# Performance work log

Measured on AMD Instinct MI355X. Metric: run time of the kernel, lower is better.

The kernel has to match this reference:

```python
import jax, jax.numpy as jnp
import numpy as np

D, P, H, FF, HD = 1024, 512, 16, 4096, 64
B, L = 2, 1024
EPS = 1e-5


def rotate_half(x):
    x1, x2 = jnp.split(x, 2, axis=-1)
    return jnp.concatenate([-x2, x1], axis=-1)


def apply_rope(x, pos):  # x: [B,H,L,HD], pos: [L,HD] angles
    c = jnp.cos(pos)[None, None]
    s = jnp.sin(pos)[None, None]
    return x * c + rotate_half(x) * s


def layer_norm(x, g, b):
    mu = jnp.mean(x, axis=-1, keepdims=True)
    var = jnp.var(x, axis=-1, keepdims=True)
    return (x - mu) * jax.lax.rsqrt(var + EPS) * g + b


def heads(x):  # [B,L,D] -> [B,H,L,HD]
    Bq, Lq, _ = x.shape
    return x.reshape(Bq, Lq, H, HD).transpose(0, 2, 1, 3)


def attention(q, k, v, alibi, pos, mask):
    if pos is not None:
        q = apply_rope(q, pos)
        k = apply_rope(k, pos)
    scores = jnp.einsum('bhqd,bhkd->bhqk', q, k) * (HD ** -0.5)
    scores = jnp.where(mask[:, None, None, :], -jnp.inf, scores)
    scores = scores + alibi[None]
    w = jax.nn.softmax(scores, axis=-1)
    out = jnp.einsum('bhqk,bhkd->bhqd', w, v)
    return out.transpose(0, 2, 1, 3).reshape(out.shape[0], out.shape[2], D)


def setup_inputs() -> dict:
    key = jax.random.key(0)
    ks = iter(jax.random.split(key, 64))

    def rn(shape, scale=1.0):
        return jax.random.normal(next(ks), shape, dtype=jnp.float32) * scale

    inp = {
        'memory': rn((B, L, D)),
        'tgt': rn((B, L, D)),
        'self_alibi_bias': rn((H, L, L)),
        'self_pos_emb': rn((L, HD)),
        'cross_alibi_bias': rn((H, L, L)),
        'cross_pos_emb': rn((L, HD)),
        'mask': jax.random.randint(next(ks), (B, L), 0, 2) > 0,
        # self attention params
        'sa_lat_w': rn((D, P), 0.02), 'sa_lat_b': jnp.zeros((P,)),
        'sa_q_w': rn((P, D), 0.02), 'sa_q_b': jnp.zeros((D,)),
        'sa_k_w': rn((P, D), 0.02), 'sa_k_b': jnp.zeros((D,)),
        'sa_v_w': rn((P, D), 0.02), 'sa_v_b': jnp.zeros((D,)),
        'sa_out_w': rn((D, D), 0.02), 'sa_out_b': jnp.zeros((D,)),
        # cross attention params
        'ca_lat_w': rn((D, P), 0.02), 'ca_lat_b': jnp.zeros((P,)),
        'ca_q_w': rn((D, D), 0.02), 'ca_q_b': jnp.zeros((D,)),
        'ca_k_w': rn((P, D), 0.02), 'ca_k_b': jnp.zeros((D,)),
        'ca_v_w': rn((P, D), 0.02), 'ca_v_b': jnp.zeros((D,)),
        'ca_out_w': rn((D, D), 0.02), 'ca_out_b': jnp.zeros((D,)),
        # ffn + norms
        'lin1_w': rn((D, FF), 0.02), 'lin1_b': jnp.zeros((FF,)),
        'lin2_w': rn((FF, D), 0.02), 'lin2_b': jnp.zeros((D,)),
        'n1_g': jnp.ones((D,)), 'n1_b': jnp.zeros((D,)),
        'n2_g': jnp.ones((D,)), 'n2_b': jnp.zeros((D,)),
        'n3_g': jnp.ones((D,)), 'n3_b': jnp.zeros((D,)),
    }
    return inp


def reference(memory, tgt, self_alibi_bias, self_pos_emb, cross_alibi_bias,
              cross_pos_emb, mask,
              sa_lat_w, sa_lat_b, sa_q_w, sa_q_b, sa_k_w, sa_k_b,
              sa_v_w, sa_v_b, sa_out_w, sa_out_b,
              ca_lat_w, ca_lat_b, ca_q_w, ca_q_b, ca_k_w, ca_k_b,
              ca_v_w, ca_v_b, ca_out_w, ca_out_b,
              lin1_w, lin1_b, lin2_w, lin2_b,
              n1_g, n1_b, n2_g, n2_b, n3_g, n3_b):
    # self attention (q,k,v all from latent projection of tgt)
    proj = tgt @ sa_lat_w + sa_lat_b                      # [B,L,P]
    q = heads(proj @ sa_q_w + sa_q_b)
    k = heads(proj @ sa_k_w + sa_k_b)
    v = heads(proj @ sa_v_w + sa_v_b)
    sa = attention(q, k, v, self_alibi_bias, self_pos_emb, mask)
    sa = sa @ sa_out_w + sa_out_b
    x = tgt + layer_norm(sa, n1_g, n1_b)

    # cross attention (q from current tgt stream, k/v from latent of memory)
    mproj = memory @ ca_lat_w + ca_lat_b                  # [B,L,P]
    q = heads(x @ ca_q_w + ca_q_b)
    k = heads(mproj @ ca_k_w + ca_k_b)
    v = heads(mproj @ ca_v_w + ca_v_b)
    ca = attention(q, k, v, cross_alibi_bias, cross_pos_emb, mask)
    ca = ca @ ca_out_w + ca_out_b
    x = x + layer_norm(ca, n2_g, n2_b)

    # FFN
    f = jax.nn.gelu(x @ lin1_w + lin1_b, approximate=False) @ lin2_w + lin2_b
    x = layer_norm(x + f, n3_g, n3_b)
    return x
```

## Files before the change

kernel.cpp:

```cpp
#include <hip/hip_runtime.h>
#include <hip/hip_bf16.h>
#include <math.h>

typedef __hip_bfloat16 hbf16;
typedef __attribute__((ext_vector_type(8))) short bf16x8;
typedef __attribute__((ext_vector_type(4))) float f32x4;

constexpr int kD  = 1024;
constexpr int kP  = 512;
constexpr int kH  = 16;
constexpr int kFF = 4096;
constexpr int kHD = 64;
constexpr int kB  = 2;
constexpr int kL  = 1024;
constexpr int kTok = kB * kL;

__device__ inline short f2bf(float x) { hbf16 h = __float2bfloat16(x); return *(short*)&h; }

__device__ __forceinline__ void gload16(const void* g, void* l) {
    __builtin_amdgcn_global_load_lds(
        (const __attribute__((address_space(1))) void*)g,
        (__attribute__((address_space(3))) void*)l, 16, 0, 0);
}

__global__ __launch_bounds__(256) void cast_bf16(
    const float* __restrict__ in, short* __restrict__ out, int total4)
{
    int i = blockIdx.x * 256 + threadIdx.x;
    if (i >= total4) return;
    float4 v = *(const float4*)&in[(size_t)i * 4];
    *(short4*)&out[(size_t)i * 4] = make_short4(f2bf(v.x), f2bf(v.y), f2bf(v.z), f2bf(v.w));
}

__global__ __launch_bounds__(256) void transpose_bf16(
    const float* __restrict__ src, short* __restrict__ dst, int K, int N)
{
    __shared__ float t[32][33];
    int n0 = blockIdx.x * 32, k0 = blockIdx.y * 32;
    int tx = threadIdx.x & 31, ty = threadIdx.x >> 5;
    #pragma unroll
    for (int r = ty; r < 32; r += 8)
        t[r][tx] = src[(size_t)(k0 + r) * N + n0 + tx];
    __syncthreads();
    #pragma unroll
    for (int r = ty; r < 32; r += 8)
        dst[(size_t)(n0 + r) * K + k0 + tx] = f2bf(t[tx][r]);
}

__global__ __launch_bounds__(256) void bias_fill(
    const float* __restrict__ bias, float* __restrict__ C, int N, int total4)
{
    int i = blockIdx.x * 256 + threadIdx.x;
    if (i >= total4) return;
    int n = (i * 4) & (N - 1);
    *(float4*)&C[(size_t)i * 4] = *(const float4*)&bias[n];
}

__global__ void concat_bias(float* __restrict__ o, const float* __restrict__ a,
                            const float* __restrict__ b, const float* __restrict__ c, int n)
{
    int i = blockIdx.x * blockDim.x + threadIdx.x;
    if (i < n) o[i] = a[i];
    else if (i < 2 * n) { if (b) o[i] = b[i - n]; }
    else if (i < 3 * n) { if (c) o[i] = c[i - 2 * n]; }
}

__global__ __launch_bounds__(256) void gemm_mfma(
    const short* __restrict__ A, const short* __restrict__ WT,
    const float* __restrict__ bias, float* __restrict__ C, short* __restrict__ C16,
    int M, int N, int K, int act, int ksplit)
{
    __shared__ short As[128 * 32];
    __shared__ short Bs[128 * 32];
    const int tid = threadIdx.x;

    const int gx = gridDim.x;
    const int nwg = gx * gridDim.y;
    const int orig = blockIdx.y * gx + blockIdx.x;
    const int qq = nwg >> 3, rr = nwg & 7;
    const int xcd = orig & 7, lid = orig >> 3;
    const int swz = (xcd < rr) ? (xcd * (qq + 1) + lid)
                               : (rr * (qq + 1) + (xcd - rr) * qq + lid);
    const int m0 = (swz / gx) * 128, n0 = (swz % gx) * 128;

    const int ks = K / ksplit;
    const int kbeg = blockIdx.z * ks, kend = kbeg + ks;
    const int wave = tid >> 6, lane = tid & 63;
    const int l15 = lane & 15, quad = lane >> 4;
    const int wm = (wave & 1) * 64, wn = (wave >> 1) * 64;

    const int srow = wave * 32 + (lane >> 2);
    const int scol = (lane & 3) * 8;

    f32x4 acc[4][4];
    #pragma unroll
    for (int i = 0; i < 4; ++i)
        #pragma unroll
        for (int j = 0; j < 4; ++j)
            acc[i][j] = (f32x4){0.f, 0.f, 0.f, 0.f};

    for (int kk = kbeg; kk < kend; kk += 32) {
        gload16(&A [(size_t)(m0 + srow) * K + kk + scol],      &As[wave * 1024]);
        gload16(&A [(size_t)(m0 + srow + 16) * K + kk + scol], &As[wave * 1024 + 512]);
        gload16(&WT[(size_t)(n0 + srow) * K + kk + scol],      &Bs[wave * 1024]);
        gload16(&WT[(size_t)(n0 + srow + 16) * K + kk + scol], &Bs[wave * 1024 + 512]);
        __syncthreads();

        bf16x8 af[4], bfr[4];
        #pragma unroll
        for (int i = 0; i < 4; ++i)
            af[i] = *(bf16x8*)&As[(wm + i * 16 + l15) * 32 + quad * 8];
        #pragma unroll
        for (int j = 0; j < 4; ++j)
            bfr[j] = *(bf16x8*)&Bs[(wn + j * 16 + l15) * 32 + quad * 8];
        #pragma unroll
        for (int i = 0; i < 4; ++i)
            #pragma unroll
            for (int j = 0; j < 4; ++j)
                acc[i][j] = __builtin_amdgcn_mfma_f32_16x16x32_bf16(af[i], bfr[j], acc[i][j], 0, 0, 0);
        __syncthreads();
    }

    #pragma unroll
    for (int j = 0; j < 4; ++j) {
        int n = n0 + wn + j * 16 + l15;
        if (ksplit == 1) {
            float bv = bias[n];
            #pragma unroll
            for (int i = 0; i < 4; ++i) {
                int mb = m0 + wm + i * 16 + quad * 4;
                #pragma unroll
                for (int r = 0; r < 4; ++r) {
                    float v = acc[i][j][r] + bv;
                    if (act) v = v * 0.5f * (1.0f + erff(v * 0.70710678118654752f));
                    if (C)   C[(size_t)(mb + r) * N + n] = v;
                    if (C16) C16[(size_t)(mb + r) * N + n] = f2bf(v);
                }
            }
        } else {
            #pragma unroll
            for (int i = 0; i < 4; ++i) {
                int mb = m0 + wm + i * 16 + quad * 4;
                #pragma unroll
                for (int r = 0; r < 4; ++r)
                    atomicAdd(&C[(size_t)(mb + r) * N + n], acc[i][j][r]);
            }
        }
    }
}

__global__ void qk_pack(const float* __restrict__ x, const float* __restrict__ pos,
                        short* __restrict__ outp, float scale, int ldx, int off)
{
    int idx = blockIdx.x * blockDim.x + threadIdx.x;
    if (idx >= kTok * kH * 32) return;
    int d = idx & 31;
    int h = (idx >> 5) & (kH - 1);
    int row = idx >> 9;
    int l = row & (kL - 1);
    int b = row >> 10;
    float a1 = pos[l * kHD + d];
    float a2 = pos[l * kHD + d + 32];
    size_t base = (size_t)row * ldx + off + h * kHD;
    float x1 = x[base + d], x2 = x[base + d + 32];
    float r1 = (x1 * cosf(a1) - x2 * sinf(a1)) * scale;
    float r2 = (x2 * cosf(a2) + x1 * sinf(a2)) * scale;
    size_t ob = ((size_t)(b * kH + h) * kL + l) * 64;
    outp[ob + d]      = f2bf(r1);
    outp[ob + d + 32] = f2bf(r2);
}

__global__ __launch_bounds__(256) void v_pack(const float* __restrict__ v, short* __restrict__ outp,
                                              int ldx, int off)
{
    int l0 = blockIdx.x * 64, h = blockIdx.y, b = blockIdx.z;
    __shared__ float t[64][65];
    int tid = threadIdx.x;
    #pragma unroll
    for (int e = 0; e < 4; ++e) {
        int idx = tid + e * 256;
        int r = idx >> 4, c4 = (idx & 15) * 4;
        const float4 vv = *(const float4*)&v[(size_t)(b * kL + l0 + r) * ldx + off + h * kHD + c4];
        t[r][c4] = vv.x; t[r][c4 + 1] = vv.y; t[r][c4 + 2] = vv.z; t[r][c4 + 3] = vv.w;
    }
    __syncthreads();
    int hd = tid >> 2, seg = (tid & 3) * 16;
    size_t ob = ((size_t)(b * kH + h) * 64 + hd) * kL + l0 + seg;
    short tmp[16];
    #pragma unroll
    for (int i = 0; i < 16; ++i) tmp[i] = f2bf(t[seg + i][hd]);
    #pragma unroll
    for (int i = 0; i < 16; i += 4)
        *(short4*)&outp[ob + i] = make_short4(tmp[i], tmp[i + 1], tmp[i + 2], tmp[i + 3]);
}

constexpr int AQ = 64, AK = 64;
__global__ __launch_bounds__(256, 2) void attn_mfma(
    const short* __restrict__ qpk, const short* __restrict__ kpk,
    const short* __restrict__ vpk, const float* __restrict__ alibi,
    const int* __restrict__ mask, short* __restrict__ out)
{
    const int q0 = blockIdx.x * AQ, h = blockIdx.y, b = blockIdx.z;
    const int tid = threadIdx.x, wave = tid >> 6, lane = tid & 63;
    const int l15 = lane & 15, quad = lane >> 4;
    __shared__ short Qf[4096];
    __shared__ short Kf[4096];
    __shared__ short Vf[4096];
    __shared__ float ALPS[4 * 1088];

    const short* qbase = qpk + ((size_t)(b * kH + h) * kL) * 64;
    const short* kbase = kpk + ((size_t)(b * kH + h) * kL) * 64;
    const short* vbase = vpk + ((size_t)(b * kH + h) * 64) * kL;
    const float* abase = alibi + ((size_t)h * kL + q0) * kL;
    const int*   mbase = mask + b * kL;

    const int sr = tid >> 3, sc8 = (tid & 7) * 8;
    const int sQuad = (sc8 >> 3) & 3, sS = sc8 >> 5;
    const int ar = tid >> 4, ac4 = (tid & 15) * 4;

    #pragma unroll
    for (int e = 0; e < 2; ++e) {
        int r = sr + e * 32;
        int slot = ((r >> 4) * 2 + sS) * 512 + (r & 15) * 32 + sQuad * 8;
        *(bf16x8*)&Qf[slot] = *(const bf16x8*)&qbase[(size_t)(q0 + r) * 64 + sc8];
    }

    bf16x8 rk[2], rv[2];
    float4 ral[4];
    int4 rmk;
    auto load_tile = [&](int k0) {
        #pragma unroll
        for (int e = 0; e < 2; ++e) {
            int r = sr + e * 32;
            rk[e] = *(const bf16x8*)&kbase[(size_t)(k0 + r) * 64 + sc8];
            rv[e] = *(const bf16x8*)&vbase[(size_t)r * kL + k0 + sc8];
        }
        #pragma unroll
        for (int e = 0; e < 4; ++e)
            ral[e] = *(const float4*)&abase[(size_t)(ar + e * 16) * kL + k0 + ac4];
        rmk = *(const int4*)&mbase[k0 + ac4];
    };
    auto store_tile = [&]() {
        #pragma unroll
        for (int e = 0; e < 2; ++e) {
            int r = sr + e * 32;
            int slot = ((r >> 4) * 2 + sS) * 512 + (r & 15) * 32 + sQuad * 8;
            *(bf16x8*)&Kf[slot] = rk[e];
            *(bf16x8*)&Vf[slot] = rv[e];
        }
        #pragma unroll
        for (int e = 0; e < 4; ++e) {
            float4 a = ral[e];
            a.x = rmk.x ? -1e30f : a.x;
            a.y = rmk.y ? -1e30f : a.y;
            a.z = rmk.z ? -1e30f : a.z;
            a.w = rmk.w ? -1e30f : a.w;
            *(float4*)&ALPS[(ar + e * 16) * 68 + ac4] = a;
        }
    };

    float mst[4], lst[4];
    #pragma unroll
    for (int r = 0; r < 4; ++r) { mst[r] = -3e38f; lst[r] = 0.f; }
    f32x4 oacc[4];
    #pragma unroll
    for (int j = 0; j < 4; ++j) oacc[j] = (f32x4){0.f, 0.f, 0.f, 0.f};

    load_tile(0);
    __syncthreads();

    bf16x8 aq[2];
    #pragma unroll
    for (int s = 0; s < 2; ++s)
        aq[s] = *(bf16x8*)&Qf[(wave * 2 + s) * 512 + l15 * 32 + quad * 8];

    for (int t = 0; t < kL / AK; ++t) {
        store_tile();
        __syncthreads();
        if (t + 1 < kL / AK) load_tile((t + 1) * AK);

        f32x4 sacc[4];
        #pragma unroll
        for (int nt = 0; nt < 4; ++nt) sacc[nt] = (f32x4){0.f, 0.f, 0.f, 0.f};
        #pragma unroll
        for (int nt = 0; nt < 4; ++nt)
            #pragma unroll
            for (int s = 0; s < 2; ++s) {
                bf16x8 bk = *(bf16x8*)&Kf[(nt * 2 + s) * 512 + l15 * 32 + quad * 8];
                sacc[nt] = __builtin_amdgcn_mfma_f32_16x16x32_bf16(aq[s], bk, sacc[nt], 0, 0, 0);
            }

        float sv[4][4];
        float mx[4] = {-3e38f, -3e38f, -3e38f, -3e38f};
        #pragma unroll
        for (int nt = 0; nt < 4; ++nt)
            #pragma unroll
            for (int r = 0; r < 4; ++r) {
                float al = ALPS[(wave * 16 + quad * 4 + r) * 68 + nt * 16 + l15];
                float s = sacc[nt][r] + al;
                sv[nt][r] = s;
                mx[r] = fmaxf(mx[r], s);
            }
        #pragma unroll
        for (int m = 1; m <= 8; m <<= 1)
            #pragma unroll
            for (int r = 0; r < 4; ++r)
                mx[r] = fmaxf(mx[r], __shfl_xor(mx[r], m));
        float alpha[4], lsum[4];
        #pragma unroll
        for (int r = 0; r < 4; ++r) {
            float mn = fmaxf(mst[r], mx[r]);
            alpha[r] = __expf(mst[r] - mn);
            mst[r] = mn;
            lsum[r] = 0.f;
        }
        #pragma unroll
        for (int nt = 0; nt < 4; ++nt)
            #pragma unroll
            for (int r = 0; r < 4; ++r) {
                float p = __expf(sv[nt][r] - mst[r]);
                sv[nt][r] = p;
                lsum[r] += p;
            }
        #pragma unroll
        for (int m = 1; m <= 8; m <<= 1)
            #pragma unroll
            for (int r = 0; r < 4; ++r)
                lsum[r] += __shfl_xor(lsum[r], m);
        #pragma unroll
        for (int r = 0; r < 4; ++r) lst[r] = lst[r] * alpha[r] + lsum[r];

        #pragma unroll
        for (int nt = 0; nt < 4; ++nt)
            #pragma unroll
            for (int r = 0; r < 4; ++r)
                ALPS[wave * 1088 + (quad * 4 + r) * 67 + nt * 16 + l15] = sv[nt][r];
        #pragma unroll
        for (int j = 0; j < 4; ++j)
            #pragma unroll
            for (int r = 0; r < 4; ++r)
                oacc[j][r] *= alpha[r];

        #pragma unroll
        for (int s = 0; s < 2; ++s) {
            int pb = wave * 1088 + l15 * 67 + s * 32 + quad * 8;
            bf16x8 ap;
            #pragma unroll
            for (int e = 0; e < 8; ++e) ap[e] = f2bf(ALPS[pb + e]);
            #pragma unroll
            for (int j = 0; j < 4; ++j) {
                bf16x8 bv = *(bf16x8*)&Vf[(j * 2 + s) * 512 + l15 * 32 + quad * 8];
                oacc[j] = __builtin_amdgcn_mfma_f32_16x16x32_bf16(ap, bv, oacc[j], 0, 0, 0);
            }
        }
        __syncthreads();
    }

    #pragma unroll
    for (int j = 0; j < 4; ++j)
        #pragma unroll
        for (int r = 0; r < 4; ++r) {
            int qrow = q0 + wave * 16 + quad * 4 + r;
            out[(size_t)(b * kL + qrow) * kD + h * kHD + j * 16 + l15] = f2bf(oacc[j][r] / lst[r]);
        }
}

__global__ __launch_bounds__(256) void add_ln(
    const float* __restrict__ res, const float* __restrict__ z,
    const float* __restrict__ g, const float* __restrict__ bi,
    float* __restrict__ out, short* __restrict__ out16)
{
    int row = blockIdx.x, tid = threadIdx.x;
    __shared__ float red[256], red2[256];
    const float* zr = z + (size_t)row * kD;
    float s = 0.f, sq = 0.f;
    for (int i = tid; i < kD; i += 256) { float vv = zr[i]; s += vv; sq += vv * vv; }
    red[tid] = s; red2[tid] = sq; __syncthreads();
    for (int st = 128; st > 0; st >>= 1) {
        if (tid < st) { red[tid] += red[tid + st]; red2[tid] += red2[tid + st]; }
        __syncthreads();
    }
    float mean = red[0] / kD;
    float var = red2[0] / kD - mean * mean;
    float rstd = rsqrtf(var + 1e-5f);
    for (int i = tid; i < kD; i += 256) {
        float vv = (zr[i] - mean) * rstd * g[i] + bi[i];
        float o = res[(size_t)row * kD + i] + vv;
        out[(size_t)row * kD + i] = o;
        out16[(size_t)row * kD + i] = f2bf(o);
    }
}

__global__ __launch_bounds__(256) void ln_final(
    const float* __restrict__ res, const float* __restrict__ f,
    const float* __restrict__ g, const float* __restrict__ bi,
    float* __restrict__ out)
{
    int row = blockIdx.x, tid = threadIdx.x;
    __shared__ float tt[kD];
    __shared__ float red[256], red2[256];
    float s = 0.f, sq = 0.f;
    for (int i = tid; i < kD; i += 256) {
        float vv = res[(size_t)row * kD + i] + f[(size_t)row * kD + i];
        tt[i] = vv; s += vv; sq += vv * vv;
    }
    red[tid] = s; red2[tid] = sq; __syncthreads();
    for (int st = 128; st > 0; st >>= 1) {
        if (tid < st) { red[tid] += red[tid + st]; red2[tid] += red2[tid + st]; }
        __syncthreads();
    }
    float mean = red[0] / kD;
    float var = red2[0] / kD - mean * mean;
    float rstd = rsqrtf(var + 1e-5f);
    for (int i = tid; i < kD; i += 256)
        out[(size_t)row * kD + i] = (tt[i] - mean) * rstd * g[i] + bi[i];
}

extern "C" void kernel_launch(void* const* d_in, const int* in_sizes, int n_in,
                              void* d_out, int out_size, void* d_ws, size_t ws_size,
                              hipStream_t stream)
{
    const float* memory      = (const float*)d_in[0];
    const float* tgt         = (const float*)d_in[1];
    const float* self_alibi  = (const float*)d_in[2];
    const float* self_pos    = (const float*)d_in[3];
    const float* cross_alibi = (const float*)d_in[4];
    const float* cross_pos   = (const float*)d_in[5];
    const int*   mask        = (const int*)d_in[6];
    const float* sa_lat_w = (const float*)d_in[7];   const float* sa_lat_b = (const float*)d_in[8];
    const float* sa_q_w   = (const float*)d_in[9];   const float* sa_q_b   = (const float*)d_in[10];
    const float* sa_k_w   = (const float*)d_in[11];  const float* sa_k_b   = (const float*)d_in[12];
    const float* sa_v_w   = (const float*)d_in[13];  const float* sa_v_b   = (const float*)d_in[14];
    const float* sa_out_w = (const float*)d_in[15];  const float* sa_out_b = (const float*)d_in[16];
    const float* ca_lat_w = (const float*)d_in[17];  const float* ca_lat_b = (const float*)d_in[18];
    const float* ca_q_w   = (const float*)d_in[19];  const float* ca_q_b   = (const float*)d_in[20];
    const float* ca_k_w   = (const float*)d_in[21];  const float* ca_k_b   = (const float*)d_in[22];
    const float* ca_v_w   = (const float*)d_in[23];  const float* ca_v_b   = (const float*)d_in[24];
    const float* ca_out_w = (const float*)d_in[25];  const float* ca_out_b = (const float*)d_in[26];
    const float* lin1_w   = (const float*)d_in[27];  const float* lin1_b   = (const float*)d_in[28];
    const float* lin2_w   = (const float*)d_in[29];  const float* lin2_b   = (const float*)d_in[30];
    const float* n1_g = (const float*)d_in[31];  const float* n1_b = (const float*)d_in[32];
    const float* n2_g = (const float*)d_in[33];  const float* n2_b = (const float*)d_in[34];
    const float* n3_g = (const float*)d_in[35];  const float* n3_b = (const float*)d_in[36];

    const size_t M1 = 1u << 20;
    float* W      = (float*)d_ws;
    float* xb     = W;
    short* tgt16  = (short*)W;
    float* tmp    = W + 2 * M1;
    short* mem16  = (short*)(W + 2 * M1);
    short* xb16   = (short*)(W + 4 * M1);
    float* proj   = W + 5 * M1;
    short* qpk    = (short*)(W + 5 * M1);
    short* proj16 = (short*)(W + 6 * M1);
    float* qkvb   = W + 6 * M1 + M1 / 2;
    short* attnb16= (short*)(W + 6 * M1 + M1 / 2);
    short* ffh16  = (short*)(W + 7 * M1 + M1 / 2);
    short* wslot  = (short*)(W + 12 * M1 + M1 / 2);
    short* kpk    = (short*)(W + 12 * M1 + M1 / 2);
    short* vpk    = (short*)(W + 13 * M1 + M1 / 2);
    float* bcat   = W + 14 * M1 + M1 / 2;

    auto gemm = [&](const short* A, const float* Wt, const float* bias, float* C, short* C16,
                    int M, int N, int K, int act, int S) {
        transpose_bf16<<<dim3(N / 32, K / 32), dim3(256), 0, stream>>>(Wt, wslot, K, N);
        if (S > 1)
            bias_fill<<<dim3(M * N / 1024), dim3(256), 0, stream>>>(bias, C, N, M * N / 4);
        gemm_mfma<<<dim3(N / 128, M / 128, S), dim3(256), 0, stream>>>(A, wslot, bias, C, C16, M, N, K, act, S);
    };
    dim3 agrid(kL / AQ, kH, kB);
    dim3 vgrid(kL / 64, kH, kB);
    dim3 tgD(kD / 32, kP / 32);

    cast_bf16<<<dim3(2048), dim3(256), 0, stream>>>(tgt, tgt16, kTok * kD / 4);
    gemm(tgt16, sa_lat_w, sa_lat_b, proj, nullptr, kTok, kP, kD, 0, 4);
    cast_bf16<<<dim3(1024), dim3(256), 0, stream>>>(proj, proj16, kTok * kP / 4);
    transpose_bf16<<<tgD, dim3(256), 0, stream>>>(sa_q_w, wslot, kP, kD);
    transpose_bf16<<<tgD, dim3(256), 0, stream>>>(sa_k_w, wslot + (size_t)kD * kP, kP, kD);
    transpose_bf16<<<tgD, dim3(256), 0, stream>>>(sa_v_w, wslot + (size_t)2 * kD * kP, kP, kD);
    concat_bias<<<dim3(12), dim3(256), 0, stream>>>(bcat, sa_q_b, sa_k_b, sa_v_b, kD);
    gemm_mfma<<<dim3(3 * kD / 128, kTok / 128, 1), dim3(256), 0, stream>>>(
        proj16, wslot, bcat, qkvb, nullptr, kTok, 3 * kD, kP, 0, 1);
    qk_pack<<<dim3(4096), dim3(256), 0, stream>>>(qkvb, self_pos, qpk, 0.125f, 3 * kD, 0);
    qk_pack<<<dim3(4096), dim3(256), 0, stream>>>(qkvb, self_pos, kpk, 1.0f, 3 * kD, kD);
    v_pack<<<vgrid, dim3(256), 0, stream>>>(qkvb, vpk, 3 * kD, 2 * kD);
    attn_mfma<<<agrid, dim3(256), 0, stream>>>(qpk, kpk, vpk, self_alibi, mask, attnb16);
    gemm(attnb16, sa_out_w, sa_out_b, tmp, nullptr, kTok, kD, kD, 0, 2);
    add_ln<<<dim3(kTok), dim3(256), 0, stream>>>(tgt, tmp, n1_g, n1_b, xb, xb16);

    cast_bf16<<<dim3(2048), dim3(256), 0, stream>>>(memory, mem16, kTok * kD / 4);
    gemm(mem16, ca_lat_w, ca_lat_b, proj, nullptr, kTok, kP, kD, 0, 4);
    cast_bf16<<<dim3(1024), dim3(256), 0, stream>>>(proj, proj16, kTok * kP / 4);
    float* qb  = qkvb;
    float* kvb = qkvb + 2 * M1;
    gemm(xb16, ca_q_w, ca_q_b, qb, nullptr, kTok, kD, kD, 0, 2);
    transpose_bf16<<<tgD, dim3(256), 0, stream>>>(ca_k_w, wslot, kP, kD);
    transpose_bf16<<<tgD, dim3(256), 0, stream>>>(ca_v_w, wslot + (size_t)kD * kP, kP, kD);
    concat_bias<<<dim3(8), dim3(256), 0, stream>>>(bcat, ca_k_b, ca_v_b, nullptr, kD);
    gemm_mfma<<<dim3(2 * kD / 128, kTok / 128, 1), dim3(256), 0, stream>>>(
        proj16, wslot, bcat, kvb, nullptr, kTok, 2 * kD, kP, 0, 1);
    qk_pack<<<dim3(4096), dim3(256), 0, stream>>>(qb, cross_pos, qpk, 0.125f, kD, 0);
    qk_pack<<<dim3(4096), dim3(256), 0, stream>>>(kvb, cross_pos, kpk, 1.0f, 2 * kD, 0);
    v_pack<<<vgrid, dim3(256), 0, stream>>>(kvb, vpk, 2 * kD, kD);
    attn_mfma<<<agrid, dim3(256), 0, stream>>>(qpk, kpk, vpk, cross_alibi, mask, attnb16);
    gemm(attnb16, ca_out_w, ca_out_b, tmp, nullptr, kTok, kD, kD, 0, 2);
    add_ln<<<dim3(kTok), dim3(256), 0, stream>>>(xb, tmp, n2_g, n2_b, xb, xb16);

    gemm(xb16, lin1_w, lin1_b, nullptr, ffh16, kTok, kFF, kD, 1, 1);
    gemm(ffh16, lin2_w, lin2_b, tmp, nullptr, kTok, kD, kFF, 0, 4);
    ln_final<<<dim3(kTok), dim3(256), 0, stream>>>(xb, tmp, n3_g, n3_b, (float*)d_out);
}
```

Baseline: 693.7 us.

## Double-buffer GEMM LDS tiles and use fragment-ordered layout for conflict-free reads

The bf16 MFMA GEMM now keeps two LDS buffers and issues global-to-LDS loads for the next k-slice before doing the MFMAs on the current one, so memory latency can overlap with compute and one barrier per iteration is removed. The staging layout is also reorganised so each 16-row group is stored in fragment order, letting every lane read its bf16x8 at a contiguous lane*8 offset to avoid LDS bank conflicts. This doubles LDS usage (32 KB per block), which may reduce occupancy, and it relies on the single remaining barrier to order the buffer reuse correctly.

```diff
diff --git a/kernel.cpp b/kernel.cpp
--- a/kernel.cpp
+++ b/kernel.cpp
@@ -70,8 +70,8 @@
     const float* __restrict__ bias, float* __restrict__ C, short* __restrict__ C16,
     int M, int N, int K, int act, int ksplit)
 {
-    __shared__ short As[128 * 32];
-    __shared__ short Bs[128 * 32];
+    __shared__ short As[2][4096];
+    __shared__ short Bs[2][4096];
     const int tid = threadIdx.x;
 
     const int gx = gridDim.x;
@@ -89,8 +89,12 @@
     const int l15 = lane & 15, quad = lane >> 4;
     const int wm = (wave & 1) * 64, wn = (wave >> 1) * 64;
 
-    const int srow = wave * 32 + (lane >> 2);
-    const int scol = (lane & 3) * 8;
+    const int sgr = lane & 15;
+    const int sgq = (lane >> 4) * 8;
+    const size_t arow0 = (size_t)(m0 + wave * 32 + sgr) * K + sgq;
+    const size_t arow1 = arow0 + (size_t)16 * K;
+    const size_t brow0 = (size_t)(n0 + wave * 32 + sgr) * K + sgq;
+    const size_t brow1 = brow0 + (size_t)16 * K;
 
     f32x4 acc[4][4];
     #pragma unroll
@@ -99,26 +103,37 @@
         for (int j = 0; j < 4; ++j)
             acc[i][j] = (f32x4){0.f, 0.f, 0.f, 0.f};
 
+    gload16(&A [arow0 + kbeg], &As[0][(wave * 2) * 512]);
+    gload16(&A [arow1 + kbeg], &As[0][(wave * 2 + 1) * 512]);
+    gload16(&WT[brow0 + kbeg], &Bs[0][(wave * 2) * 512]);
+    gload16(&WT[brow1 + kbeg], &Bs[0][(wave * 2 + 1) * 512]);
+    __syncthreads();
+
+    const int ga = (wave & 1) * 4, gb = (wave >> 1) * 4;
+    int cur = 0;
     for (int kk = kbeg; kk < kend; kk += 32) {
-        gload16(&A [(size_t)(m0 + srow) * K + kk + scol],      &As[wave * 1024]);
-        gload16(&A [(size_t)(m0 + srow + 16) * K + kk + scol], &As[wave * 1024 + 512]);
-        gload16(&WT[(size_t)(n0 + srow) * K + kk + scol],      &Bs[wave * 1024]);
-        gload16(&WT[(size_t)(n0 + srow + 16) * K + kk + scol], &Bs[wave * 1024 + 512]);
-        __syncthreads();
+        if (kk + 32 < kend) {
+            int nxt = cur ^ 1;
+            gload16(&A [arow0 + kk + 32], &As[nxt][(wave * 2) * 512]);
+            gload16(&A [arow1 + kk + 32], &As[nxt][(wave * 2 + 1) * 512]);
+            gload16(&WT[brow0 + kk + 32], &Bs[nxt][(wave * 2) * 512]);
+            gload16(&WT[brow1 + kk + 32], &Bs[nxt][(wave * 2 + 1) * 512]);
+        }
 
         bf16x8 af[4], bfr[4];
         #pragma unroll
         for (int i = 0; i < 4; ++i)
-            af[i] = *(bf16x8*)&As[(wm + i * 16 + l15) * 32 + quad * 8];
+            af[i] = *(bf16x8*)&As[cur][(ga + i) * 512 + lane * 8];
         #pragma unroll
         for (int j = 0; j < 4; ++j)
-            bfr[j] = *(bf16x8*)&Bs[(wn + j * 16 + l15) * 32 + quad * 8];
+            bfr[j] = *(bf16x8*)&Bs[cur][(gb + j) * 512 + lane * 8];
         #pragma unroll
         for (int i = 0; i < 4; ++i)
             #pragma unroll
             for (int j = 0; j < 4; ++j)
                 acc[i][j] = __builtin_amdgcn_mfma_f32_16x16x32_bf16(af[i], bfr[j], acc[i][j], 0, 0, 0);
         __syncthreads();
+        cur ^= 1;
     }
 
     #pragma unroll
```

Result: slower. 710.3 us (+2.4%).

## Pipeline GEMM global-to-LDS loads with a four-stage ring buffer

Applied to the files above, without the earlier changes.

Replaces the single-buffered LDS tiles in the MFMA GEMM with a 4-deep ring of A/B tiles. Loads for later k-steps are issued ahead of time, and waits use explicit vmcnt counts so memory latency overlaps with MFMA work. The LDS layout also changes so each 16-row fragment is stored contiguously per lane, which avoids strided reads. This quadruples LDS use per block, which may cut occupancy, and it relies on hand-written waitcnt and barrier sequencing.

```diff
diff --git a/kernel.cpp b/kernel.cpp
--- a/kernel.cpp
+++ b/kernel.cpp
@@ -70,8 +70,8 @@
     const float* __restrict__ bias, float* __restrict__ C, short* __restrict__ C16,
     int M, int N, int K, int act, int ksplit)
 {
-    __shared__ short As[128 * 32];
-    __shared__ short Bs[128 * 32];
+    __shared__ short As[4][4096];
+    __shared__ short Bs[4][4096];
     const int tid = threadIdx.x;
 
     const int gx = gridDim.x;
@@ -84,13 +84,18 @@
     const int m0 = (swz / gx) * 128, n0 = (swz % gx) * 128;
 
     const int ks = K / ksplit;
-    const int kbeg = blockIdx.z * ks, kend = kbeg + ks;
+    const int kbeg = blockIdx.z * ks;
+    const int nt = ks / 32;
     const int wave = tid >> 6, lane = tid & 63;
     const int l15 = lane & 15, quad = lane >> 4;
     const int wm = (wave & 1) * 64, wn = (wave >> 1) * 64;
 
-    const int srow = wave * 32 + (lane >> 2);
-    const int scol = (lane & 3) * 8;
+    const int sgr = lane & 15;
+    const int sgq = (lane >> 4) * 8;
+    const size_t arow0 = (size_t)(m0 + wave * 32 + sgr) * K + sgq + kbeg;
+    const size_t arow1 = arow0 + (size_t)16 * K;
+    const size_t brow0 = (size_t)(n0 + wave * 32 + sgr) * K + sgq + kbeg;
+    const size_t brow1 = brow0 + (size_t)16 * K;
 
     f32x4 acc[4][4];
     #pragma unroll
@@ -99,26 +104,45 @@
         for (int j = 0; j < 4; ++j)
             acc[i][j] = (f32x4){0.f, 0.f, 0.f, 0.f};
 
-    for (int kk = kbeg; kk < kend; kk += 32) {
-        gload16(&A [(size_t)(m0 + srow) * K + kk + scol],      &As[wave * 1024]);
-        gload16(&A [(size_t)(m0 + srow + 16) * K + kk + scol], &As[wave * 1024 + 512]);
-        gload16(&WT[(size_t)(n0 + srow) * K + kk + scol],      &Bs[wave * 1024]);
-        gload16(&WT[(size_t)(n0 + srow + 16) * K + kk + scol], &Bs[wave * 1024 + 512]);
-        __syncthreads();
-
+    auto issue = [&](int t) {
+        int bi = t & 3;
+        int koff = t * 32;
+        gload16(&A [arow0 + koff], &As[bi][(wave * 2) * 512]);
+        gload16(&A [arow1 + koff], &As[bi][(wave * 2 + 1) * 512]);
+        gload16(&WT[brow0 + koff], &Bs[bi][(wave * 2) * 512]);
+        gload16(&WT[brow1 + koff], &Bs[bi][(wave * 2 + 1) * 512]);
+    };
+
+    issue(0); issue(1); issue(2); issue(3);
+
+    const int ga = (wave & 1) * 4, gb = (wave >> 1) * 4;
+    for (int t = 0; t < nt; ++t) {
+        int ahead = nt - 1 - t; if (ahead > 3) ahead = 3;
+        if (ahead == 3)      asm volatile("s_waitcnt vmcnt(12)" ::: "memory");
+        else if (ahead == 2) asm volatile("s_waitcnt vmcnt(8)"  ::: "memory");
+        else if (ahead == 1) asm volatile("s_waitcnt vmcnt(4)"  ::: "memory");
+        else                 asm volatile("s_waitcnt vmcnt(0)"  ::: "memory");
+        __builtin_amdgcn_sched_barrier(0);
+        __builtin_amdgcn_s_barrier();
+
+        int bi = t & 3;
         bf16x8 af[4], bfr[4];
         #pragma unroll
         for (int i = 0; i < 4; ++i)
-            af[i] = *(bf16x8*)&As[(wm + i * 16 + l15) * 32 + quad * 8];
+            af[i] = *(bf16x8*)&As[bi][(ga + i) * 512 + lane * 8];
         #pragma unroll
         for (int j = 0; j < 4; ++j)
-            bfr[j] = *(bf16x8*)&Bs[(wn + j * 16 + l15) * 32 + quad * 8];
+            bfr[j] = *(bf16x8*)&Bs[bi][(gb + j) * 512 + lane * 8];
         #pragma unroll
         for (int i = 0; i < 4; ++i)
             #pragma unroll
             for (int j = 0; j < 4; ++j)
                 acc[i][j] = __builtin_amdgcn_mfma_f32_16x16x32_bf16(af[i], bfr[j], acc[i][j], 0, 0, 0);
-        __syncthreads();
+
+        asm volatile("s_waitcnt lgkmcnt(0)" ::: "memory");
+        __builtin_amdgcn_sched_barrier(0);
+        __builtin_amdgcn_s_barrier();
+        if (t + 4 < nt) issue(t + 4);
     }
 
     #pragma unroll
```

After: 710.2 us. 2.4% more time.
